# Optimization experiments

Measured on AMD Instinct MI355X. Metric: run time of the kernel, lower is better.

Reference implementation:

```python
import jax, jax.numpy as jnp
import numpy as np

B, NVIS, NHID, NCLASS = 2048, 2048, 1024, 64


def setup_inputs() -> dict:
    key = jax.random.key(0)
    k1, k2, k3, k4, k5 = jax.random.split(key, 5)
    return {
        "v": jax.random.normal(k1, (B, NVIS), dtype=jnp.float32),
        "W": jax.random.normal(k2, (NVIS, NHID), dtype=jnp.float32),
        "c": jax.random.normal(k3, (1, NHID), dtype=jnp.float32),
        "d": jax.random.normal(k4, (1, NCLASS), dtype=jnp.float32),
        "U": jax.random.normal(k5, (NCLASS, NHID), dtype=jnp.float32),
    }


def reference(v, W, c, d, U):
    # precomputed_factor: [B, nhid]
    pre = jnp.matmul(v, W) + c
    # class free energies F[b, y] = d[0, y] + sum_j softplus(pre[b, j] + U[y, j])
    # broadcast to [B, nclass, nhid], reduce over hidden units
    F = d[0] + jnp.sum(jax.nn.softplus(pre[:, None, :] + U[None, :, :]), axis=-1)  # [B, nclass]
    # pairwise normalization 1 / sum_d exp(F_d - F_c) == softmax(F) along classes
    class_probs = jax.nn.softmax(F, axis=1)
    max_idx = jnp.argmax(class_probs, axis=1)
    one_hot = jax.nn.one_hot(max_idx, U.shape[0], dtype=jnp.int32)
    return class_probs, one_hot
```

## Files before the change

### kernel.cpp

```cpp
#include <hip/hip_runtime.h>

constexpr int kB    = 2048;
constexpr int kVIS  = 2048;
constexpr int kHID  = 1024;
constexpr int kCLS  = 64;
constexpr float kLog2e = 1.4426950408889634f;

typedef __attribute__((ext_vector_type(8))) short bf16x8;
typedef __attribute__((ext_vector_type(4))) float f32x4;
typedef __attribute__((ext_vector_type(2))) float f32x2;

typedef __attribute__((address_space(3))) unsigned       as3_u32;
typedef __attribute__((address_space(1))) const unsigned as1_u32;

__device__ __forceinline__ void g2lds16(const void* g, void* l) {
    __builtin_amdgcn_global_load_lds((as1_u32*)g, (as3_u32*)l, 16, 0, 0);
}

__device__ __forceinline__ unsigned short f2bf(float x) {
    unsigned u = __float_as_uint(x);
    u += 0x7fffu + ((u >> 16) & 1u);
    return (unsigned short)(u >> 16);
}
__device__ __forceinline__ float bf2f(unsigned short h) {
    return __uint_as_float(((unsigned)h) << 16);
}

__global__ __launch_bounds__(256) void prep_all(const float* __restrict__ v,
                                                const float* __restrict__ W,
                                                const float* __restrict__ U,
                                                unsigned short* __restrict__ vh,
                                                unsigned short* __restrict__ vl,
                                                unsigned short* __restrict__ wth,
                                                unsigned short* __restrict__ wtl,
                                                float* __restrict__ Utp) {
    __shared__ float T[32][33];
    const int bx = blockIdx.x;
    if (bx < 4096) {
        const int i = (bx * 256 + threadIdx.x) * 4;
        const float4 xv = *(const float4*)(v + i);
        ushort4 h, l;
        h.x = f2bf(xv.x); l.x = f2bf(xv.x - bf2f(h.x));
        h.y = f2bf(xv.y); l.y = f2bf(xv.y - bf2f(h.y));
        h.z = f2bf(xv.z); l.z = f2bf(xv.z - bf2f(h.z));
        h.w = f2bf(xv.w); l.w = f2bf(xv.w - bf2f(h.w));
        *(ushort4*)(vh + i) = h;
        *(ushort4*)(vl + i) = l;
    } else if (bx < 6144) {
        const int b = bx - 4096;
        const int n0 = (b & 31) * 32, k0 = (b >> 5) * 32;
        const int c = threadIdx.x & 31, r0 = threadIdx.x >> 5;
#pragma unroll
        for (int p = 0; p < 4; ++p) {
            const int r = r0 + p * 8;
            T[r][c] = W[(size_t)(k0 + r) * kHID + n0 + c];
        }
        __syncthreads();
#pragma unroll
        for (int p = 0; p < 4; ++p) {
            const int rr = r0 + p * 8;
            const float x = T[c][rr];
            const unsigned short h = f2bf(x);
            const unsigned short l = f2bf(x - bf2f(h));
            const size_t o = (size_t)(n0 + rr) * kVIS + k0 + c;
            wth[o] = h;
            wtl[o] = l;
        }
    } else {
        const int id = (bx - 6144) * 256 + threadIdx.x;
        const int j = id >> 6, y = id & 63;
        Utp[(((j >> 2) * kCLS + y) << 2) + (j & 3)] = U[(size_t)y * kHID + j] * kLog2e;
    }
}

__global__ __launch_bounds__(256) void gemm_fused(const unsigned short* __restrict__ vh,
                                                  const unsigned short* __restrict__ vl,
                                                  const unsigned short* __restrict__ wth,
                                                  const unsigned short* __restrict__ wtl,
                                                  const float* __restrict__ cvec,
                                                  const float* __restrict__ Utp,
                                                  float* __restrict__ Fpart) {
    __shared__ __align__(16) union SMem {
        unsigned short stage[2][4][64 * 64];
        float psH[2][64][68];
    } smem;

    const int tid = threadIdx.x;
    const int lane = tid & 63, wave = tid >> 6;
    const int mh = wave >> 1;
    const int kh = wave & 1;

    const int bid = blockIdx.x;
    const int idx = bid >> 3;
    const int mstripe = ((bid & 7) << 2) + (idx >> 4);
    const int ncol = idx & 15;
    const int m0 = mstripe * 64, n0 = ncol * 64;

    const int r0 = tid >> 3, r1 = r0 + 32;
    const int oc = (((tid & 7) ^ ((tid >> 3) & 7)) << 3);
    const size_t ga0 = (size_t)(m0 + r0) * kVIS + oc;
    const size_t ga1 = (size_t)(m0 + r1) * kVIS + oc;
    const size_t gb0 = (size_t)(n0 + r0) * kVIS + oc;
    const size_t gb1 = (size_t)(n0 + r1) * kVIS + oc;
    const int l0 = (r0 << 6) + ((tid & 7) << 3);
    const int l1 = (r1 << 6) + ((tid & 7) << 3);

    const int fm = lane & 15, fq = lane >> 4;
    const int rx = fm & 7;
    const int ar0 = (mh * 32 + fm) << 6, ar1 = (mh * 32 + 16 + fm) << 6;
    const int br0 = (fm) << 6,      br1 = (16 + fm) << 6;
    const int br2 = (32 + fm) << 6, br3 = (48 + fm) << 6;
    const int p = (((kh << 2) + fq) ^ rx) << 3;

    f32x4 acc[2][4] = {};

    {
        unsigned short* Ah = smem.stage[0][0];
        unsigned short* Al = smem.stage[0][1];
        unsigned short* Bh = smem.stage[0][2];
        unsigned short* Bl = smem.stage[0][3];
        g2lds16(vh + ga0, Ah + l0);  g2lds16(vh + ga1, Ah + l1);
        g2lds16(vl + ga0, Al + l0);  g2lds16(vl + ga1, Al + l1);
        g2lds16(wth + gb0, Bh + l0); g2lds16(wth + gb1, Bh + l1);
        g2lds16(wtl + gb0, Bl + l0); g2lds16(wtl + gb1, Bl + l1);
    }
    __syncthreads();

    int cur = 0;
    for (int k0 = 0; k0 < kVIS; k0 += 64) {
        if (k0 + 64 < kVIS) {
            unsigned short* Ah = smem.stage[cur ^ 1][0];
            unsigned short* Al = smem.stage[cur ^ 1][1];
            unsigned short* Bh = smem.stage[cur ^ 1][2];
            unsigned short* Bl = smem.stage[cur ^ 1][3];
            const int ko = k0 + 64;
            g2lds16(vh + ga0 + ko, Ah + l0);  g2lds16(vh + ga1 + ko, Ah + l1);
            g2lds16(vl + ga0 + ko, Al + l0);  g2lds16(vl + ga1 + ko, Al + l1);
            g2lds16(wth + gb0 + ko, Bh + l0); g2lds16(wth + gb1 + ko, Bh + l1);
            g2lds16(wtl + gb0 + ko, Bl + l0); g2lds16(wtl + gb1 + ko, Bl + l1);
        }
        const unsigned short* Ah = smem.stage[cur][0];
        const unsigned short* Al = smem.stage[cur][1];
        const unsigned short* Bh = smem.stage[cur][2];
        const unsigned short* Bl = smem.stage[cur][3];
        const bf16x8 a_h0 = *(const bf16x8*)(Ah + ar0 + p);
        const bf16x8 a_h1 = *(const bf16x8*)(Ah + ar1 + p);
        const bf16x8 a_l0 = *(const bf16x8*)(Al + ar0 + p);
        const bf16x8 a_l1 = *(const bf16x8*)(Al + ar1 + p);
        const bf16x8 b_h0 = *(const bf16x8*)(Bh + br0 + p);
        const bf16x8 b_h1 = *(const bf16x8*)(Bh + br1 + p);
        const bf16x8 b_h2 = *(const bf16x8*)(Bh + br2 + p);
        const bf16x8 b_h3 = *(const bf16x8*)(Bh + br3 + p);
        const bf16x8 b_l0 = *(const bf16x8*)(Bl + br0 + p);
        const bf16x8 b_l1 = *(const bf16x8*)(Bl + br1 + p);
        const bf16x8 b_l2 = *(const bf16x8*)(Bl + br2 + p);
        const bf16x8 b_l3 = *(const bf16x8*)(Bl + br3 + p);
        acc[0][0] = __builtin_amdgcn_mfma_f32_16x16x32_bf16(a_h0, b_h0, acc[0][0], 0, 0, 0);
        acc[0][0] = __builtin_amdgcn_mfma_f32_16x16x32_bf16(a_h0, b_l0, acc[0][0], 0, 0, 0);
        acc[0][0] = __builtin_amdgcn_mfma_f32_16x16x32_bf16(a_l0, b_h0, acc[0][0], 0, 0, 0);
        acc[0][1] = __builtin_amdgcn_mfma_f32_16x16x32_bf16(a_h0, b_h1, acc[0][1], 0, 0, 0);
        acc[0][1] = __builtin_amdgcn_mfma_f32_16x16x32_bf16(a_h0, b_l1, acc[0][1], 0, 0, 0);
        acc[0][1] = __builtin_amdgcn_mfma_f32_16x16x32_bf16(a_l0, b_h1, acc[0][1], 0, 0, 0);
        acc[0][2] = __builtin_amdgcn_mfma_f32_16x16x32_bf16(a_h0, b_h2, acc[0][2], 0, 0, 0);
        acc[0][2] = __builtin_amdgcn_mfma_f32_16x16x32_bf16(a_h0, b_l2, acc[0][2], 0, 0, 0);
        acc[0][2] = __builtin_amdgcn_mfma_f32_16x16x32_bf16(a_l0, b_h2, acc[0][2], 0, 0, 0);
        acc[0][3] = __builtin_amdgcn_mfma_f32_16x16x32_bf16(a_h0, b_h3, acc[0][3], 0, 0, 0);
        acc[0][3] = __builtin_amdgcn_mfma_f32_16x16x32_bf16(a_h0, b_l3, acc[0][3], 0, 0, 0);
        acc[0][3] = __builtin_amdgcn_mfma_f32_16x16x32_bf16(a_l0, b_h3, acc[0][3], 0, 0, 0);
        acc[1][0] = __builtin_amdgcn_mfma_f32_16x16x32_bf16(a_h1, b_h0, acc[1][0], 0, 0, 0);
        acc[1][0] = __builtin_amdgcn_mfma_f32_16x16x32_bf16(a_h1, b_l0, acc[1][0], 0, 0, 0);
        acc[1][0] = __builtin_amdgcn_mfma_f32_16x16x32_bf16(a_l1, b_h0, acc[1][0], 0, 0, 0);
        acc[1][1] = __builtin_amdgcn_mfma_f32_16x16x32_bf16(a_h1, b_h1, acc[1][1], 0, 0, 0);
        acc[1][1] = __builtin_amdgcn_mfma_f32_16x16x32_bf16(a_h1, b_l1, acc[1][1], 0, 0, 0);
        acc[1][1] = __builtin_amdgcn_mfma_f32_16x16x32_bf16(a_l1, b_h1, acc[1][1], 0, 0, 0);
        acc[1][2] = __builtin_amdgcn_mfma_f32_16x16x32_bf16(a_h1, b_h2, acc[1][2], 0, 0, 0);
        acc[1][2] = __builtin_amdgcn_mfma_f32_16x16x32_bf16(a_h1, b_l2, acc[1][2], 0, 0, 0);
        acc[1][2] = __builtin_amdgcn_mfma_f32_16x16x32_bf16(a_l1, b_h2, acc[1][2], 0, 0, 0);
        acc[1][3] = __builtin_amdgcn_mfma_f32_16x16x32_bf16(a_h1, b_h3, acc[1][3], 0, 0, 0);
        acc[1][3] = __builtin_amdgcn_mfma_f32_16x16x32_bf16(a_h1, b_l3, acc[1][3], 0, 0, 0);
        acc[1][3] = __builtin_amdgcn_mfma_f32_16x16x32_bf16(a_l1, b_h3, acc[1][3], 0, 0, 0);
        __syncthreads();
        cur ^= 1;
    }

#pragma unroll
    for (int j = 0; j < 4; ++j) {
        const int col = j * 16 + fm;
        const float cadd = kh ? 0.f : cvec[n0 + col];
#pragma unroll
        for (int i = 0; i < 2; ++i) {
            const int rbase = mh * 32 + i * 16 + fq * 4;
#pragma unroll
            for (int r = 0; r < 4; ++r)
                smem.psH[kh][rbase + r][col] = (acc[i][j][r] + cadd) * kLog2e;
        }
    }
    __syncthreads();

    const int q0 = (n0 >> 2);
    f32x2 relu2[16], prod2[16];
#pragma unroll
    for (int rr = 0; rr < 16; ++rr) { relu2[rr] = (f32x2)(0.f); prod2[rr] = (f32x2)(1.f); }

    const f32x2 zero2 = (f32x2)(0.f);
    for (int jc = 0; jc < 64; jc += 8) {
        const float4 ua = ((const float4*)Utp)[(q0 + (jc >> 2) + 0) * kCLS + lane];
        const float4 ub = ((const float4*)Utp)[(q0 + (jc >> 2) + 1) * kCLS + lane];
        const f32x2 u01 = {ua.x, ua.y}, u23 = {ua.z, ua.w};
        const f32x2 u45 = {ub.x, ub.y}, u67 = {ub.z, ub.w};
#pragma unroll
        for (int rr = 0; rr < 16; ++rr) {
            const int row = wave * 16 + rr;
            const float4 pa0 = *(const float4*)&smem.psH[0][row][jc];
            const float4 pa1 = *(const float4*)&smem.psH[0][row][jc + 4];
            const float4 pb0 = *(const float4*)&smem.psH[1][row][jc];
            const float4 pb1 = *(const float4*)&smem.psH[1][row][jc + 4];
            f32x2 tp[4];
            tp[0] = (f32x2){pa0.x + pb0.x, pa0.y + pb0.y} + u01;
            tp[1] = (f32x2){pa0.z + pb0.z, pa0.w + pb0.w} + u23;
            tp[2] = (f32x2){pa1.x + pb1.x, pa1.y + pb1.y} + u45;
            tp[3] = (f32x2){pa1.z + pb1.z, pa1.w + pb1.w} + u67;
#pragma unroll
            for (int g = 0; g < 4; ++g) {
                const f32x2 t = tp[g];
                f32x2 e;
                e.x = __builtin_amdgcn_exp2f(-__builtin_fabsf(t.x));
                e.y = __builtin_amdgcn_exp2f(-__builtin_fabsf(t.y));
                prod2[rr] = __builtin_elementwise_fma(prod2[rr], e, prod2[rr]);
                relu2[rr] += __builtin_elementwise_max(t, zero2);
            }
        }
    }
#pragma unroll
    for (int rr = 0; rr < 16; ++rr) {
        const float contrib = relu2[rr].x + relu2[rr].y +
                              __builtin_amdgcn_logf(prod2[rr].x * prod2[rr].y);
        Fpart[((size_t)ncol * kB + m0 + wave * 16 + rr) * kCLS + lane] = contrib;
    }
}

__global__ __launch_bounds__(256) void softmax_final(const float* __restrict__ Fpart,
                                                     const float* __restrict__ dvec,
                                                     float* __restrict__ out) {
    const int tid = threadIdx.x;
    const int lane = tid & 63, wave = tid >> 6;
    const int row = blockIdx.x * 4 + wave;
    double s = 0.0;
#pragma unroll
    for (int k = 0; k < kHID / 64; ++k)
        s += (double)Fpart[((size_t)k * kB + row) * kCLS + lane];
    const float G = (float)s + dvec[lane] * kLog2e;

    float m = G;
    int mi = lane;
#pragma unroll
    for (int off = 32; off; off >>= 1) {
        const float om = __shfl_xor(m, off);
        const int   oi = __shfl_xor(mi, off);
        if (om > m || (om == m && oi < mi)) { m = om; mi = oi; }
    }
    const float e2 = __builtin_amdgcn_exp2f(G - m);
    float ssum = e2;
#pragma unroll
    for (int off = 32; off; off >>= 1) ssum += __shfl_xor(ssum, off);
    out[(size_t)row * kCLS + lane] = e2 / ssum;
    out[(size_t)kB * kCLS + (size_t)row * kCLS + lane] = (lane == mi) ? 1.0f : 0.0f;
}

constexpr int BM = 64, BN = 64, BK = 16;

__global__ __launch_bounds__(256) void gemm_vw(const float* __restrict__ V,
                                               const float* __restrict__ Wm,
                                               const float* __restrict__ cvec,
                                               float* __restrict__ pre) {
    __shared__ float As[BK][BM + 4];
    __shared__ float Bs[BK][BN + 4];
    const int tid = threadIdx.x;
    const int tx = tid & 15, ty = tid >> 4;
    const int m0 = blockIdx.y * BM, n0 = blockIdx.x * BN;
    const int arow = tid >> 2, acol = (tid & 3) << 2;
    const int brow = tid >> 4, bcol = (tid & 15) << 2;
    const float* vptr = V + (size_t)(m0 + arow) * kVIS + acol;
    const float* wptr = Wm + (size_t)brow * kHID + n0 + bcol;
    float acc[4][4] = {};
    for (int k0 = 0; k0 < kVIS; k0 += BK) {
        const float4 a4 = *(const float4*)(vptr + k0);
        const float4 b4 = *(const float4*)(wptr + (size_t)k0 * kHID);
        __syncthreads();
        As[acol + 0][arow] = a4.x; As[acol + 1][arow] = a4.y;
        As[acol + 2][arow] = a4.z; As[acol + 3][arow] = a4.w;
        *(float4*)&Bs[brow][bcol] = b4;
        __syncthreads();
#pragma unroll
        for (int k = 0; k < BK; ++k) {
            const float4 av = *(const float4*)&As[k][ty << 2];
            const float4 bv = *(const float4*)&Bs[k][tx << 2];
            const float a[4] = {av.x, av.y, av.z, av.w};
            const float b[4] = {bv.x, bv.y, bv.z, bv.w};
#pragma unroll
            for (int i = 0; i < 4; ++i)
#pragma unroll
                for (int j = 0; j < 4; ++j) acc[i][j] += a[i] * b[j];
        }
    }
#pragma unroll
    for (int i = 0; i < 4; ++i) {
        const int row = m0 + (ty << 2) + i;
        const int col = n0 + (tx << 2);
        const float4 cv = *(const float4*)(cvec + col);
        float4 o;
        o.x = acc[i][0] + cv.x; o.y = acc[i][1] + cv.y;
        o.z = acc[i][2] + cv.z; o.w = acc[i][3] + cv.w;
        *(float4*)(pre + (size_t)row * kHID + col) = o;
    }
}

__device__ __forceinline__ float softplus_f(float x) {
    return fmaxf(x, 0.f) + __logf(1.f + __expf(-fabsf(x)));
}

__global__ __launch_bounds__(256) void classify(const float* __restrict__ pre,
                                                const float* __restrict__ U,
                                                const float* __restrict__ dvec,
                                                float* __restrict__ out) {
    __shared__ float preS[4][kHID];
    __shared__ float Fs[4][kCLS];
    const int tid = threadIdx.x;
    const int lane = tid & 63, wave = tid >> 6;
    const int b0 = blockIdx.x * 4;
    const float4* src = (const float4*)(pre + (size_t)b0 * kHID);
    float4* dst = (float4*)preS;
    for (int i = tid; i < kHID; i += 256) dst[i] = src[i];
    __syncthreads();
    for (int yi = 0; yi < 16; ++yi) {
        const int y = (wave << 4) + yi;
        const float* Uy = U + (size_t)y * kHID;
        float a0 = 0.f, a1 = 0.f, a2 = 0.f, a3 = 0.f;
#pragma unroll
        for (int it = 0; it < kHID / 64; ++it) {
            const int j = lane + (it << 6);
            const float u = Uy[j];
            a0 += softplus_f(preS[0][j] + u);
            a1 += softplus_f(preS[1][j] + u);
            a2 += softplus_f(preS[2][j] + u);
            a3 += softplus_f(preS[3][j] + u);
        }
        double d0 = a0, d1 = a1, d2 = a2, d3 = a3;
#pragma unroll
        for (int off = 32; off; off >>= 1) {
            d0 += __shfl_xor(d0, off); d1 += __shfl_xor(d1, off);
            d2 += __shfl_xor(d2, off); d3 += __shfl_xor(d3, off);
        }
        if (lane == 0) {
            const float dy = dvec[y];
            Fs[0][y] = (float)d0 + dy; Fs[1][y] = (float)d1 + dy;
            Fs[2][y] = (float)d2 + dy; Fs[3][y] = (float)d3 + dy;
        }
    }
    __syncthreads();
    const float F = Fs[wave][lane];
    float m = F; int mi = lane;
#pragma unroll
    for (int off = 32; off; off >>= 1) {
        const float om = __shfl_xor(m, off);
        const int oi = __shfl_xor(mi, off);
        if (om > m || (om == m && oi < mi)) { m = om; mi = oi; }
    }
    const float e = __expf(F - m);
    float s = e;
#pragma unroll
    for (int off = 32; off; off >>= 1) s += __shfl_xor(s, off);
    const int row = b0 + wave;
    out[(size_t)row * kCLS + lane] = e / s;
    out[(size_t)kB * kCLS + (size_t)row * kCLS + lane] = (lane == mi) ? 1.0f : 0.0f;
}

extern "C" void kernel_launch(void* const* d_in, const int* in_sizes, int n_in,
                              void* d_out, int out_size, void* d_ws, size_t ws_size,
                              hipStream_t stream) {
    const float* v = (const float*)d_in[0];
    const float* W = (const float*)d_in[1];
    const float* c = (const float*)d_in[2];
    const float* d = (const float*)d_in[3];
    const float* U = (const float*)d_in[4];
    float* out = (float*)d_out;
    char* ws = (char*)d_ws;

    const size_t need = 33816576;
    if (ws_size >= need) {
        unsigned short* vh  = (unsigned short*)(ws);
        unsigned short* vl  = (unsigned short*)(ws + 8388608);
        unsigned short* wth = (unsigned short*)(ws + 16777216);
        unsigned short* wtl = (unsigned short*)(ws + 20971520);
        float* Utp   = (float*)(ws + 25165824);
        float* Fpart = (float*)(ws + 25427968);
        prep_all<<<6400, 256, 0, stream>>>(v, W, U, vh, vl, wth, wtl, Utp);
        gemm_fused<<<512, 256, 0, stream>>>(vh, vl, wth, wtl, c, Utp, Fpart);
        softmax_final<<<kB / 4, 256, 0, stream>>>(Fpart, d, out);
    } else {
        float* pre = (float*)ws;
        gemm_vw<<<dim3(kHID / BN, kB / BM), 256, 0, stream>>>(v, W, c, pre);
        classify<<<kB / 4, 256, 0, stream>>>(pre, U, d, out);
    }
}
```

Baseline: 134.7 us.

## Use 512 threads per block in fused GEMM, splitting N across wave pairs

Doubles the fused GEMM block to 8 waves. Each wave now computes a 32x32 sub-tile (M half, N half, K half) instead of 32x64, and each thread issues one async global-to-LDS load per matrix instead of two. The softmax-energy epilogue is split so each wave handles 8 rows instead of 16. The aim is more waves per CU and fewer registers per thread to hide latency, at the cost of fewer MFMAs per LDS fragment load and more waves contending at each barrier.

```diff
diff --git a/kernel.cpp b/kernel.cpp
--- a/kernel.cpp
+++ b/kernel.cpp
@@ -73,13 +73,13 @@
     }
 }
 
-__global__ __launch_bounds__(256) void gemm_fused(const unsigned short* __restrict__ vh,
-                                                  const unsigned short* __restrict__ vl,
-                                                  const unsigned short* __restrict__ wth,
-                                                  const unsigned short* __restrict__ wtl,
-                                                  const float* __restrict__ cvec,
-                                                  const float* __restrict__ Utp,
-                                                  float* __restrict__ Fpart) {
+__global__ __launch_bounds__(512, 4) void gemm_fused(const unsigned short* __restrict__ vh,
+                                                     const unsigned short* __restrict__ vl,
+                                                     const unsigned short* __restrict__ wth,
+                                                     const unsigned short* __restrict__ wtl,
+                                                     const float* __restrict__ cvec,
+                                                     const float* __restrict__ Utp,
+                                                     float* __restrict__ Fpart) {
     __shared__ __align__(16) union SMem {
         unsigned short stage[2][4][64 * 64];
         float psH[2][64][68];
@@ -87,7 +87,8 @@
 
     const int tid = threadIdx.x;
     const int lane = tid & 63, wave = tid >> 6;
-    const int mh = wave >> 1;
+    const int mh = wave >> 2;
+    const int nh = (wave >> 1) & 1;
     const int kh = wave & 1;
 
     const int bid = blockIdx.x;
@@ -96,48 +97,36 @@
     const int ncol = idx & 15;
     const int m0 = mstripe * 64, n0 = ncol * 64;
 
-    const int r0 = tid >> 3, r1 = r0 + 32;
+    const int r = tid >> 3;
     const int oc = (((tid & 7) ^ ((tid >> 3) & 7)) << 3);
-    const size_t ga0 = (size_t)(m0 + r0) * kVIS + oc;
-    const size_t ga1 = (size_t)(m0 + r1) * kVIS + oc;
-    const size_t gb0 = (size_t)(n0 + r0) * kVIS + oc;
-    const size_t gb1 = (size_t)(n0 + r1) * kVIS + oc;
-    const int l0 = (r0 << 6) + ((tid & 7) << 3);
-    const int l1 = (r1 << 6) + ((tid & 7) << 3);
+    const size_t ga = (size_t)(m0 + r) * kVIS + oc;
+    const size_t gb = (size_t)(n0 + r) * kVIS + oc;
+    const int ls = (r << 6) + ((tid & 7) << 3);
 
     const int fm = lane & 15, fq = lane >> 4;
     const int rx = fm & 7;
     const int ar0 = (mh * 32 + fm) << 6, ar1 = (mh * 32 + 16 + fm) << 6;
-    const int br0 = (fm) << 6,      br1 = (16 + fm) << 6;
-    const int br2 = (32 + fm) << 6, br3 = (48 + fm) << 6;
+    const int br0 = (nh * 32 + fm) << 6, br1 = (nh * 32 + 16 + fm) << 6;
     const int p = (((kh << 2) + fq) ^ rx) << 3;
 
-    f32x4 acc[2][4] = {};
+    f32x4 acc[2][2] = {};
 
     {
-        unsigned short* Ah = smem.stage[0][0];
-        unsigned short* Al = smem.stage[0][1];
-        unsigned short* Bh = smem.stage[0][2];
-        unsigned short* Bl = smem.stage[0][3];
-        g2lds16(vh + ga0, Ah + l0);  g2lds16(vh + ga1, Ah + l1);
-        g2lds16(vl + ga0, Al + l0);  g2lds16(vl + ga1, Al + l1);
-        g2lds16(wth + gb0, Bh + l0); g2lds16(wth + gb1, Bh + l1);
-        g2lds16(wtl + gb0, Bl + l0); g2lds16(wtl + gb1, Bl + l1);
+        g2lds16(vh + ga,  smem.stage[0][0] + ls);
+        g2lds16(vl + ga,  smem.stage[0][1] + ls);
+        g2lds16(wth + gb, smem.stage[0][2] + ls);
+        g2lds16(wtl + gb, smem.stage[0][3] + ls);
     }
     __syncthreads();
 
     int cur = 0;
     for (int k0 = 0; k0 < kVIS; k0 += 64) {
         if (k0 + 64 < kVIS) {
-            unsigned short* Ah = smem.stage[cur ^ 1][0];
-            unsigned short* Al = smem.stage[cur ^ 1][1];
-            unsigned short* Bh = smem.stage[cur ^ 1][2];
-            unsigned short* Bl = smem.stage[cur ^ 1][3];
             const int ko = k0 + 64;
-            g2lds16(vh + ga0 + ko, Ah + l0);  g2lds16(vh + ga1 + ko, Ah + l1);
-            g2lds16(vl + ga0 + ko, Al + l0);  g2lds16(vl + ga1 + ko, Al + l1);
-            g2lds16(wth + gb0 + ko, Bh + l0); g2lds16(wth + gb1 + ko, Bh + l1);
-            g2lds16(wtl + gb0 + ko, Bl + l0); g2lds16(wtl + gb1 + ko, Bl + l1);
+            g2lds16(vh + ga + ko,  smem.stage[cur ^ 1][0] + ls);
+            g2lds16(vl + ga + ko,  smem.stage[cur ^ 1][1] + ls);
+            g2lds16(wth + gb + ko, smem.stage[cur ^ 1][2] + ls);
+            g2lds16(wtl + gb + ko, smem.stage[cur ^ 1][3] + ls);
         }
         const unsigned short* Ah = smem.stage[cur][0];
         const unsigned short* Al = smem.stage[cur][1];
@@ -149,58 +138,42 @@
         const bf16x8 a_l1 = *(const bf16x8*)(Al + ar1 + p);
         const bf16x8 b_h0 = *(const bf16x8*)(Bh + br0 + p);
         const bf16x8 b_h1 = *(const bf16x8*)(Bh + br1 + p);
-        const bf16x8 b_h2 = *(const bf16x8*)(Bh + br2 + p);
-        const bf16x8 b_h3 = *(const bf16x8*)(Bh + br3 + p);
         const bf16x8 b_l0 = *(const bf16x8*)(Bl + br0 + p);
         const bf16x8 b_l1 = *(const bf16x8*)(Bl + br1 + p);
-        const bf16x8 b_l2 = *(const bf16x8*)(Bl + br2 + p);
-        const bf16x8 b_l3 = *(const bf16x8*)(Bl + br3 + p);
         acc[0][0] = __builtin_amdgcn_mfma_f32_16x16x32_bf16(a_h0, b_h0, acc[0][0], 0, 0, 0);
         acc[0][0] = __builtin_amdgcn_mfma_f32_16x16x32_bf16(a_h0, b_l0, acc[0][0], 0, 0, 0);
         acc[0][0] = __builtin_amdgcn_mfma_f32_16x16x32_bf16(a_l0, b_h0, acc[0][0], 0, 0, 0);
         acc[0][1] = __builtin_amdgcn_mfma_f32_16x16x32_bf16(a_h0, b_h1, acc[0][1], 0, 0, 0);
         acc[0][1] = __builtin_amdgcn_mfma_f32_16x16x32_bf16(a_h0, b_l1, acc[0][1], 0, 0, 0);
         acc[0][1] = __builtin_amdgcn_mfma_f32_16x16x32_bf16(a_l0, b_h1, acc[0][1], 0, 0, 0);
-        acc[0][2] = __builtin_amdgcn_mfma_f32_16x16x32_bf16(a_h0, b_h2, acc[0][2], 0, 0, 0);
-        acc[0][2] = __builtin_amdgcn_mfma_f32_16x16x32_bf16(a_h0, b_l2, acc[0][2], 0, 0, 0);
-        acc[0][2] = __builtin_amdgcn_mfma_f32_16x16x32_bf16(a_l0, b_h2, acc[0][2], 0, 0, 0);
-        acc[0][3] = __builtin_amdgcn_mfma_f32_16x16x32_bf16(a_h0, b_h3, acc[0][3], 0, 0, 0);
-        acc[0][3] = __builtin_amdgcn_mfma_f32_16x16x32_bf16(a_h0, b_l3, acc[0][3], 0, 0, 0);
-        acc[0][3] = __builtin_amdgcn_mfma_f32_16x16x32_bf16(a_l0, b_h3, acc[0][3], 0, 0, 0);
         acc[1][0] = __builtin_amdgcn_mfma_f32_16x16x32_bf16(a_h1, b_h0, acc[1][0], 0, 0, 0);
         acc[1][0] = __builtin_amdgcn_mfma_f32_16x16x32_bf16(a_h1, b_l0, acc[1][0], 0, 0, 0);
         acc[1][0] = __builtin_amdgcn_mfma_f32_16x16x32_bf16(a_l1, b_h0, acc[1][0], 0, 0, 0);
         acc[1][1] = __builtin_amdgcn_mfma_f32_16x16x32_bf16(a_h1, b_h1, acc[1][1], 0, 0, 0);
         acc[1][1] = __builtin_amdgcn_mfma_f32_16x16x32_bf16(a_h1, b_l1, acc[1][1], 0, 0, 0);
         acc[1][1] = __builtin_amdgcn_mfma_f32_16x16x32_bf16(a_l1, b_h1, acc[1][1], 0, 0, 0);
-        acc[1][2] = __builtin_amdgcn_mfma_f32_16x16x32_bf16(a_h1, b_h2, acc[1][2], 0, 0, 0);
-        acc[1][2] = __builtin_amdgcn_mfma_f32_16x16x32_bf16(a_h1, b_l2, acc[1][2], 0, 0, 0);
-        acc[1][2] = __builtin_amdgcn_mfma_f32_16x16x32_bf16(a_l1, b_h2, acc[1][2], 0, 0, 0);
-        acc[1][3] = __builtin_amdgcn_mfma_f32_16x16x32_bf16(a_h1, b_h3, acc[1][3], 0, 0, 0);
-        acc[1][3] = __builtin_amdgcn_mfma_f32_16x16x32_bf16(a_h1, b_l3, acc[1][3], 0, 0, 0);
-        acc[1][3] = __builtin_amdgcn_mfma_f32_16x16x32_bf16(a_l1, b_h3, acc[1][3], 0, 0, 0);
         __syncthreads();
         cur ^= 1;
     }
 
 #pragma unroll
-    for (int j = 0; j < 4; ++j) {
-        const int col = j * 16 + fm;
+    for (int j = 0; j < 2; ++j) {
+        const int col = nh * 32 + j * 16 + fm;
         const float cadd = kh ? 0.f : cvec[n0 + col];
 #pragma unroll
         for (int i = 0; i < 2; ++i) {
             const int rbase = mh * 32 + i * 16 + fq * 4;
 #pragma unroll
-            for (int r = 0; r < 4; ++r)
-                smem.psH[kh][rbase + r][col] = (acc[i][j][r] + cadd) * kLog2e;
+            for (int rr = 0; rr < 4; ++rr)
+                smem.psH[kh][rbase + rr][col] = (acc[i][j][rr] + cadd) * kLog2e;
         }
     }
     __syncthreads();
 
     const int q0 = (n0 >> 2);
-    f32x2 relu2[16], prod2[16];
-#pragma unroll
-    for (int rr = 0; rr < 16; ++rr) { relu2[rr] = (f32x2)(0.f); prod2[rr] = (f32x2)(1.f); }
+    f32x2 relu2[8], prod2[8];
+#pragma unroll
+    for (int rr = 0; rr < 8; ++rr) { relu2[rr] = (f32x2)(0.f); prod2[rr] = (f32x2)(1.f); }
 
     const f32x2 zero2 = (f32x2)(0.f);
     for (int jc = 0; jc < 64; jc += 8) {
@@ -209,8 +182,8 @@
         const f32x2 u01 = {ua.x, ua.y}, u23 = {ua.z, ua.w};
         const f32x2 u45 = {ub.x, ub.y}, u67 = {ub.z, ub.w};
 #pragma unroll
-        for (int rr = 0; rr < 16; ++rr) {
-            const int row = wave * 16 + rr;
+        for (int rr = 0; rr < 8; ++rr) {
+            const int row = wave * 8 + rr;
             const float4 pa0 = *(const float4*)&smem.psH[0][row][jc];
             const float4 pa1 = *(const float4*)&smem.psH[0][row][jc + 4];
             const float4 pb0 = *(const float4*)&smem.psH[1][row][jc];
@@ -232,10 +205,10 @@
         }
     }
 #pragma unroll
-    for (int rr = 0; rr < 16; ++rr) {
+    for (int rr = 0; rr < 8; ++rr) {
         const float contrib = relu2[rr].x + relu2[rr].y +
                               __builtin_amdgcn_logf(prod2[rr].x * prod2[rr].y);
-        Fpart[((size_t)ncol * kB + m0 + wave * 16 + rr) * kCLS + lane] = contrib;
+        Fpart[((size_t)ncol * kB + m0 + wave * 8 + rr) * kCLS + lane] = contrib;
     }
 }
 
@@ -395,7 +368,7 @@
         float* Utp   = (float*)(ws + 25165824);
         float* Fpart = (float*)(ws + 25427968);
         prep_all<<<6400, 256, 0, stream>>>(v, W, U, vh, vl, wth, wtl, Utp);
-        gemm_fused<<<512, 256, 0, stream>>>(vh, vl, wth, wtl, c, Utp, Fpart);
+        gemm_fused<<<512, 512, 0, stream>>>(vh, vl, wth, wtl, c, Utp, Fpart);
         softmax_final<<<kB / 4, 256, 0, stream>>>(Fpart, d, out);
     } else {
         float* pre = (float*)ws;
```

Result: faster. 130.7 us (-3.0%).
